# Kernel tuning notes

Hardware: AMD Instinct MI355X
Metric: run time of the kernel (lower is better)

The kernel has to match this reference:

```python
import jax, jax.numpy as jnp
import numpy as np

B, T, C = 4, 2048, 2048
H, HKV = 16, 4
D = C // H            # 128
G = H // HKV          # 4 query heads per kv head
ROPE_THETA = 10000.0


def _rope_tables(seq_len, head_dim, theta):
    inv = 1.0 / (theta ** (np.arange(0, head_dim, 2, dtype=np.float32) / head_dim))
    t = np.arange(seq_len, dtype=np.float32)
    f = np.outer(t, inv)  # (T, D/2)
    return jnp.asarray(np.cos(f)), jnp.asarray(np.sin(f))


def setup_inputs() -> dict:
    key = jax.random.key(0)
    ks = jax.random.split(key, 5)
    x = jax.random.normal(ks[0], (B, T, C), dtype=jnp.float32)
    W_q = jax.random.normal(ks[1], (H * D, C), dtype=jnp.float32) * 0.02
    W_k = jax.random.normal(ks[2], (HKV * D, C), dtype=jnp.float32) * 0.02
    W_v = jax.random.normal(ks[3], (HKV * D, C), dtype=jnp.float32) * 0.02
    W_o = jax.random.normal(ks[4], (C, C), dtype=jnp.float32) * 0.02
    cos, sin = _rope_tables(T, D, ROPE_THETA)
    return {"x": x, "W_q": W_q, "W_k": W_k, "W_v": W_v, "W_o": W_o,
            "cos": cos, "sin": sin}


def _apply_rope(xh, cos, sin):
    # xh: (B, h, T, D); cos/sin: (T, D/2)
    x0 = xh[..., 0::2]
    x1 = xh[..., 1::2]
    c = cos[None, None, :, :]
    s = sin[None, None, :, :]
    o0 = x0 * c - x1 * s
    o1 = x0 * s + x1 * c
    return jnp.stack([o0, o1], axis=-1).reshape(xh.shape)


def reference(x, W_q, W_k, W_v, W_o, cos, sin):
    b, t, c = x.shape
    q = (x @ W_q.T).reshape(b, t, H, D).transpose(0, 2, 1, 3)      # (B,H,T,D)
    k = (x @ W_k.T).reshape(b, t, HKV, D).transpose(0, 2, 1, 3)    # (B,HKV,T,D)
    v = (x @ W_v.T).reshape(b, t, HKV, D).transpose(0, 2, 1, 3)
    q = _apply_rope(q, cos[:t], sin[:t])
    k = _apply_rope(k, cos[:t], sin[:t])
    # GQA via reshape instead of repeat_interleave (same head ordering:
    # q head index h = kv*G + g).
    qg = q.reshape(b, HKV, G, t, D)
    scores = jnp.einsum('bkgtd,bksd->bkgts', qg, k) / jnp.sqrt(jnp.float32(D))
    causal = jnp.tril(jnp.ones((t, t), dtype=bool))
    scores = jnp.where(causal[None, None, None, :, :], scores, -jnp.inf)
    attn = jax.nn.softmax(scores, axis=-1)
    out = jnp.einsum('bkgts,bksd->bkgtd', attn, v)                 # (B,HKV,G,T,D)
    out = out.reshape(b, H, t, D).transpose(0, 2, 1, 3).reshape(b, t, c)
    return out @ W_o.T
```

## Files before the change

### kernel.cpp

```cpp
#include <hip/hip_runtime.h>
#include <cmath>

typedef __attribute__((ext_vector_type(8))) short bf16x8;
typedef __attribute__((ext_vector_type(4))) float f32x4;
typedef __attribute__((ext_vector_type(16))) float f32x16;
typedef unsigned short u16;

__device__ __forceinline__ u16 f2bf(float f) {
  union { float f; unsigned u; } x; x.f = f;
  return (u16)((x.u + 0x7FFFu + ((x.u >> 16) & 1u)) >> 16);
}

__device__ __forceinline__ unsigned cvtpk(float lo, float hi) {
  unsigned r;
  asm("v_cvt_pk_bf16_f32 %0, %1, %2" : "=v"(r) : "v"(lo), "v"(hi));
  return r;
}

__device__ __forceinline__ void gload_lds16(const void* g, void* l) {
  __builtin_amdgcn_global_load_lds((const __attribute__((address_space(1))) unsigned*)g,
                                   (__attribute__((address_space(3))) unsigned*)l,
                                   16, 0, 0);
}

__global__ __launch_bounds__(256) void cast_bf16_kernel(const float* __restrict__ in,
                                                        u16* __restrict__ out, long n) {
  long i = (long)blockIdx.x * blockDim.x + threadIdx.x;
  long stride = (long)gridDim.x * blockDim.x;
  for (long j = i * 4; j < n; j += stride * 4) {
    float4 v = *(const float4*)(in + j);
    ushort4 o;
    o.x = f2bf(v.x); o.y = f2bf(v.y); o.z = f2bf(v.z); o.w = f2bf(v.w);
    *(ushort4*)(out + j) = o;
  }
}

template <int EPI>
__global__ __launch_bounds__(512, 2) void gemm_bt256(const u16* __restrict__ A,
                                                     const u16* __restrict__ B,
                                                     void* __restrict__ outp,
                                                     int M, int N, int K,
                                                     const float* __restrict__ cosp,
                                                     const float* __restrict__ sinp,
                                                     float scale) {
  __shared__ u16 lds[65536];
  const int tid = threadIdx.x;
  const int lane = tid & 63;
  const int l16 = lane & 15, lhi = lane >> 4;
  const int w = tid >> 6;
  const int wr = w >> 2, wc = w & 3;
  const int m0 = blockIdx.y * 256;
  const int n0 = blockIdx.x * 256;

  f32x4 acc[8][4];
#pragma unroll
  for (int i = 0; i < 8; ++i)
#pragma unroll
    for (int j = 0; j < 4; ++j) acc[i][j] = (f32x4)0.0f;

  const int NT = K >> 6;

  auto stage = [&](int t, int buf) {
    const int k0 = t << 6;
    u16* Ad = lds + buf * 32768;
    u16* Bd = Ad + 16384;
#pragma unroll
    for (int j = 0; j < 4; ++j) {
      int c = tid + j * 512;
      int row = c >> 3;
      int sboff = ((c & 7) * 16) ^ ((row & 7) << 4);
      gload_lds16(A + (size_t)(m0 + row) * K + k0 + (sboff >> 1), Ad + (size_t)c * 8);
    }
#pragma unroll
    for (int j = 0; j < 4; ++j) {
      int c = tid + j * 512;
      int row = c >> 3;
      int sboff = ((c & 7) * 16) ^ ((row & 7) << 4);
      gload_lds16(B + (size_t)(n0 + row) * K + k0 + (sboff >> 1), Bd + (size_t)c * 8);
    }
  };

  stage(0, 0);
  stage(1, 1);

  for (int t = 0; t < NT; ++t) {
    const int cur = t & 1;
    if (t + 1 < NT) { asm volatile("s_waitcnt vmcnt(8)" ::: "memory"); }
    else            { asm volatile("s_waitcnt vmcnt(0)" ::: "memory"); }
    __builtin_amdgcn_s_barrier();
    const char* Ab = (const char*)(lds + cur * 32768);
    const char* Bb = (const char*)(lds + cur * 32768 + 16384);
#pragma unroll
    for (int qm = 0; qm < 2; ++qm)
#pragma unroll
      for (int qn = 0; qn < 2; ++qn) {
        bf16x8 af[4][2], bfr[2][2];
#pragma unroll
        for (int mi = 0; mi < 4; ++mi) {
          int ra = wr * 128 + qm * 64 + mi * 16 + l16;
#pragma unroll
          for (int kk = 0; kk < 2; ++kk)
            af[mi][kk] = *(const bf16x8*)(Ab + ra * 128 + ((kk * 64 + lhi * 16) ^ ((ra & 7) << 4)));
        }
#pragma unroll
        for (int ni = 0; ni < 2; ++ni) {
          int rb = wc * 64 + qn * 32 + ni * 16 + l16;
#pragma unroll
          for (int kk = 0; kk < 2; ++kk)
            bfr[ni][kk] = *(const bf16x8*)(Bb + rb * 128 + ((kk * 64 + lhi * 16) ^ ((rb & 7) << 4)));
        }
        __builtin_amdgcn_s_setprio(1);
#pragma unroll
        for (int kk = 0; kk < 2; ++kk)
#pragma unroll
          for (int mi = 0; mi < 4; ++mi)
#pragma unroll
            for (int ni = 0; ni < 2; ++ni)
              acc[qm * 4 + mi][qn * 2 + ni] = __builtin_amdgcn_mfma_f32_16x16x32_bf16(
                  af[mi][kk], bfr[ni][kk], acc[qm * 4 + mi][qn * 2 + ni], 0, 0, 0);
        __builtin_amdgcn_s_setprio(0);
      }
    asm volatile("s_waitcnt lgkmcnt(0)" ::: "memory");
    __builtin_amdgcn_s_barrier();
    if (t + 2 < NT) stage(t + 2, cur);
  }

  if (EPI == 2) {
    float* o = (float*)outp;
#pragma unroll
    for (int mi8 = 0; mi8 < 8; ++mi8)
#pragma unroll
      for (int r = 0; r < 4; ++r) {
        int row = m0 + wr * 128 + mi8 * 16 + lhi * 4 + r;
#pragma unroll
        for (int nj = 0; nj < 4; ++nj) {
          int col = n0 + wc * 64 + nj * 16 + l16;
          o[(size_t)row * N + col] = acc[mi8][nj][r];
        }
      }
  } else {
    u16* o = (u16*)outp;
    const int nheads = N >> 7;
#pragma unroll
    for (int mi8 = 0; mi8 < 8; ++mi8)
#pragma unroll
      for (int r = 0; r < 4; ++r) {
        int row = m0 + wr * 128 + mi8 * 16 + lhi * 4 + r;
        int b = row >> 11;
        int tt = row & 2047;
#pragma unroll
        for (int nj = 0; nj < 4; ++nj) {
          int col = n0 + wc * 64 + nj * 16 + l16;
          int hh = col >> 7, dd = col & 127;
          float v = acc[mi8][nj][r];
          float p = __shfl_xor(v, 1);
          float c = cosp[tt * 64 + (dd >> 1)];
          float s = sinp[tt * 64 + (dd >> 1)];
          v = (lane & 1) ? fmaf(p, s, v * c) : fmaf(v, c, -p * s);
          v *= scale;
          o[((size_t)(b * nheads + hh) * 2048 + tt) * 128 + dd] = f2bf(v);
        }
      }
  }
}

template <int EPI>
__global__ __launch_bounds__(256) void gemm_bt(const u16* __restrict__ A,
                                               const u16* __restrict__ B,
                                               void* __restrict__ outp,
                                               u16* __restrict__ vtp,
                                               int M, int N, int K,
                                               const float* __restrict__ cosp,
                                               const float* __restrict__ sinp,
                                               float scale) {
  __shared__ u16 As[128 * 64];
  __shared__ u16 Bs[128 * 64];
  const int tid = threadIdx.x;
  const int lane = tid & 63;
  const int l16 = lane & 15, lhi = lane >> 4;
  const int w = tid >> 6;
  const int wr = w >> 1, wc = w & 1;
  const int m0 = blockIdx.y * 128;
  const int n0 = blockIdx.x * 128;
  const int wbase = tid - lane;

  f32x4 acc[4][4];
#pragma unroll
  for (int i = 0; i < 4; ++i)
#pragma unroll
    for (int j = 0; j < 4; ++j) acc[i][j] = (f32x4)0.0f;

  for (int k0 = 0; k0 < K; k0 += 64) {
    __syncthreads();
#pragma unroll
    for (int j = 0; j < 4; ++j) {
      int c = tid + j * 256;
      gload_lds16(A + (size_t)(m0 + (c >> 3)) * K + k0 + (c & 7) * 8,
                  As + (size_t)(wbase + j * 256) * 8);
    }
#pragma unroll
    for (int j = 0; j < 4; ++j) {
      int c = tid + j * 256;
      gload_lds16(B + (size_t)(n0 + (c >> 3)) * K + k0 + (c & 7) * 8,
                  Bs + (size_t)(wbase + j * 256) * 8);
    }
    __syncthreads();
#pragma unroll
    for (int kk = 0; kk < 64; kk += 32) {
      bf16x8 af[4], bfr[4];
#pragma unroll
      for (int mi = 0; mi < 4; ++mi)
        af[mi] = *(const bf16x8*)&As[(wr * 64 + mi * 16 + l16) * 64 + kk + lhi * 8];
#pragma unroll
      for (int ni = 0; ni < 4; ++ni)
        bfr[ni] = *(const bf16x8*)&Bs[(wc * 64 + ni * 16 + l16) * 64 + kk + lhi * 8];
#pragma unroll
      for (int mi = 0; mi < 4; ++mi)
#pragma unroll
        for (int ni = 0; ni < 4; ++ni)
          acc[mi][ni] = __builtin_amdgcn_mfma_f32_16x16x32_bf16(af[mi], bfr[ni], acc[mi][ni], 0, 0, 0);
    }
  }

  {
    const int bx = blockIdx.x;
    if (bx < 4) {
      u16* o = (u16*)outp;
#pragma unroll
      for (int mi = 0; mi < 4; ++mi)
#pragma unroll
        for (int r = 0; r < 4; ++r) {
          int row = m0 + wr * 64 + mi * 16 + lhi * 4 + r;
          int b = row >> 11;
          int t = row & 2047;
          size_t base = ((size_t)(b * 4 + bx) * 2048 + t) * 128;
#pragma unroll
          for (int ni = 0; ni < 4; ++ni) {
            int d = wc * 64 + ni * 16 + l16;
            float v = acc[mi][ni][r];
            float p = __shfl_xor(v, 1);
            float c = cosp[t * 64 + (d >> 1)];
            float s = sinp[t * 64 + (d >> 1)];
            v = (lane & 1) ? fmaf(p, s, v * c) : fmaf(v, c, -p * s);
            o[base + d] = f2bf(v);
          }
        }
    } else {
      const int kvh = bx - 4;
#pragma unroll
      for (int mi = 0; mi < 4; ++mi)
#pragma unroll
        for (int r = 0; r < 4; ++r) {
          int row = m0 + wr * 64 + mi * 16 + lhi * 4 + r;
          int b = row >> 11;
          int t = row & 2047;
          size_t base = ((size_t)(b * 4 + kvh) * 128) * 2048 + t;
#pragma unroll
          for (int ni = 0; ni < 4; ++ni) {
            int d = wc * 64 + ni * 16 + l16;
            vtp[base + (size_t)d * 2048] = f2bf(acc[mi][ni][r]);
          }
        }
    }
  }
}

__global__ __launch_bounds__(256, 2) void attn_kernel(const u16* __restrict__ Q,
                                                      const u16* __restrict__ Kp,
                                                      const u16* __restrict__ Vtp,
                                                      u16* __restrict__ O) {
  __shared__ u16 lds[17408];
  u16* Ks  = lds;
  u16* VTs = lds + 8192;

  const int tid = threadIdx.x;
  const int lane = tid & 63;
  const int w = tid >> 6;
  const int l5 = lane & 31, hi = lane >> 5;
  const int bid = blockIdx.x;
  const int qt = 15 - (bid >> 6);
  const int hb = bid & 63;
  const int h = hb >> 2;
  const int b = hb & 3;
  const int kvh = h >> 2;
  const int q0 = qt * 128;
  const int wbase = tid - lane;
  const int wrow0 = q0 + w * 32;
  const int qg = wrow0 + l5;

  const u16* Qb = Q + ((size_t)((b * 16 + h) * 2048 + wrow0)) * 128;
  const u16* Kb = Kp + (size_t)(b * 4 + kvh) * 2048 * 128;
  const u16* Vtb = Vtp + (size_t)(b * 4 + kvh) * 128 * 2048;

  bf16x8 qf[8];
#pragma unroll
  for (int ks = 0; ks < 8; ++ks)
    qf[ks] = *(const bf16x8*)(Qb + (size_t)l5 * 128 + ks * 16 + hi * 8);

  f32x16 oacc[4];
#pragma unroll
  for (int i = 0; i < 4; ++i) oacc[i] = (f32x16)0.0f;
  float m = -3.0e38f, l = 0.0f;

  const int nkt = 2 * qt + 2;
  for (int kt = 0; kt < nkt; ++kt) {
    const int t0 = kt * 64;
    __syncthreads();
#pragma unroll
    for (int j = 0; j < 4; ++j) {
      int c = tid + j * 256;
      int row = c >> 4;
      int sboff = ((c & 15) * 16) ^ ((row & 15) << 4);
      gload_lds16(Kb + (size_t)(t0 + row) * 128 + (sboff >> 1),
                  Ks + (size_t)(wbase + j * 256) * 8);
    }
#pragma unroll
    for (int j = 0; j < 4; ++j) {
      int c = tid + j * 256;
      int d = c >> 3;
      int sboff = ((c & 7) * 16) ^ ((d & 7) << 4);
      gload_lds16(Vtb + (size_t)d * 2048 + t0 + (sboff >> 1),
                  VTs + (size_t)(wbase + j * 256) * 8);
    }
    __syncthreads();

    if (t0 <= wrow0 + 31) {
      float p[32];
      const char* ksb = (const char*)Ks;
#pragma unroll
      for (int kt2 = 0; kt2 < 2; ++kt2) {
        f32x16 sacc = (f32x16)0.0f;
        int row = kt2 * 32 + l5;
#pragma unroll
        for (int ks = 0; ks < 8; ++ks) {
          bf16x8 kf = *(const bf16x8*)(ksb + row * 256 + ((ks * 32 + hi * 16) ^ ((row & 15) << 4)));
          sacc = __builtin_amdgcn_mfma_f32_32x32x16_bf16(kf, qf[ks], sacc, 0, 0, 0);
        }
#pragma unroll
        for (int r = 0; r < 16; ++r) p[kt2 * 16 + r] = sacc[r];
      }

      if (t0 + 63 > wrow0) {
#pragma unroll
        for (int kt2 = 0; kt2 < 2; ++kt2)
#pragma unroll
          for (int r = 0; r < 16; ++r) {
            int kvg = t0 + kt2 * 32 + (r & 3) + 8 * (r >> 2) + 4 * hi;
            if (kvg > qg) p[kt2 * 16 + r] = -3.0e38f;
          }
      }

      float mx[16];
#pragma unroll
      for (int i = 0; i < 16; ++i) mx[i] = fmaxf(p[i], p[i + 16]);
#pragma unroll
      for (int i = 0; i < 8; ++i) mx[i] = fmaxf(mx[i], mx[i + 8]);
#pragma unroll
      for (int i = 0; i < 4; ++i) mx[i] = fmaxf(mx[i], mx[i + 4]);
      float rm = fmaxf(fmaxf(mx[0], mx[1]), fmaxf(mx[2], mx[3]));
      rm = fmaxf(rm, __shfl_xor(rm, 32));

      bool defer = __all(rm <= m + 8.0f);
      if (!defer) {
        float mnew = fmaxf(m, rm);
        float sc = exp2f(m - mnew);
        m = mnew;
        l *= sc;
#pragma unroll
        for (int i = 0; i < 4; ++i)
#pragma unroll
          for (int r = 0; r < 16; ++r) oacc[i][r] *= sc;
      }

#pragma unroll
      for (int i = 0; i < 32; ++i) p[i] = exp2f(p[i] - m);
      float sm[16];
#pragma unroll
      for (int i = 0; i < 16; ++i) sm[i] = p[i] + p[i + 16];
#pragma unroll
      for (int i = 0; i < 8; ++i) sm[i] += sm[i + 8];
#pragma unroll
      for (int i = 0; i < 4; ++i) sm[i] += sm[i + 4];
      float s2 = (sm[0] + sm[1]) + (sm[2] + sm[3]);
      s2 += __shfl_xor(s2, 32);
      l += s2;

      const char* vtb = (const char*)VTs;
#pragma unroll
      for (int kt2 = 0; kt2 < 2; ++kt2) {
#pragma unroll
        for (int sl = 0; sl < 2; ++sl) {
          int base = kt2 * 16 + sl * 8;
          unsigned A0 = cvtpk(p[base + 0], p[base + 1]);
          unsigned A1 = cvtpk(p[base + 2], p[base + 3]);
          unsigned A2 = cvtpk(p[base + 4], p[base + 5]);
          unsigned A3 = cvtpk(p[base + 6], p[base + 7]);
          unsigned XA0 = __shfl_xor(A0, 32);
          unsigned XA1 = __shfl_xor(A1, 32);
          unsigned XA2 = __shfl_xor(A2, 32);
          unsigned XA3 = __shfl_xor(A3, 32);
          union { unsigned u[4]; bf16x8 v; } pf;
          pf.u[0] = hi ? XA2 : A0;
          pf.u[1] = hi ? XA3 : A1;
          pf.u[2] = hi ? A2 : XA0;
          pf.u[3] = hi ? A3 : XA1;
          int s = kt2 * 2 + sl;
#pragma unroll
          for (int dt = 0; dt < 4; ++dt) {
            int row = dt * 32 + l5;
            bf16x8 vb = *(const bf16x8*)(vtb + row * 128 + ((s * 32 + hi * 16) ^ ((row & 7) << 4)));
            oacc[dt] = __builtin_amdgcn_mfma_f32_32x32x16_bf16(vb, pf.v, oacc[dt], 0, 0, 0);
          }
        }
      }
    }
  }

  float inv = 1.0f / l;
  __syncthreads();
  u16* OS = lds + w * 4352;
#pragma unroll
  for (int dt = 0; dt < 4; ++dt)
#pragma unroll
    for (int r = 0; r < 16; ++r) {
      int d = dt * 32 + (r & 3) + 8 * (r >> 2) + 4 * hi;
      OS[l5 * 136 + d] = f2bf(oacc[dt][r] * inv);
    }
  __syncthreads();
  u16* Ob = O + ((size_t)(b * 2048 + q0)) * 2048 + h * 128;
#pragma unroll
  for (int j = 0; j < 8; ++j) {
    int c = tid + j * 256;
    int row = c >> 4, col = c & 15;
    *(bf16x8*)(Ob + (size_t)row * 2048 + col * 8) =
        *(const bf16x8*)&lds[(row >> 5) * 4352 + (row & 31) * 136 + col * 8];
  }
}

extern "C" void kernel_launch(void* const* d_in, const int* in_sizes, int n_in,
                              void* d_out, int out_size, void* d_ws, size_t ws_size,
                              hipStream_t stream) {
  (void)in_sizes; (void)n_in; (void)out_size; (void)ws_size;
  const float* x    = (const float*)d_in[0];
  const float* Wq   = (const float*)d_in[1];
  const float* Wk   = (const float*)d_in[2];
  const float* Wv   = (const float*)d_in[3];
  const float* Wo   = (const float*)d_in[4];
  const float* cosp = (const float*)d_in[5];
  const float* sinp = (const float*)d_in[6];

  u16* ws  = (u16*)d_ws;
  u16* xbf = ws;
  u16* Wqb = xbf + 16777216;
  u16* Wkb = Wqb + 4194304;
  u16* Wvb = Wkb + 1048576;
  u16* Wob = Wvb + 1048576;
  u16* Qb  = Wob + 4194304;
  u16* Kb  = Qb + 16777216;
  u16* Vb  = Kb + 4194304;
  u16* AO  = xbf;

  cast_bf16_kernel<<<2048, 256, 0, stream>>>(x,  xbf, 16777216L);
  cast_bf16_kernel<<<512,  256, 0, stream>>>(Wq, Wqb, 4194304L);
  cast_bf16_kernel<<<256,  256, 0, stream>>>(Wk, Wkb, 1048576L);
  cast_bf16_kernel<<<256,  256, 0, stream>>>(Wv, Wvb, 1048576L);
  cast_bf16_kernel<<<512,  256, 0, stream>>>(Wo, Wob, 4194304L);

  const float qscale = (float)(1.4426950408889634 / sqrt(128.0));

  gemm_bt256<0><<<dim3(8, 32), 512, 0, stream>>>(xbf, Wqb, Qb, 8192, 2048, 2048, cosp, sinp, qscale);
  gemm_bt<3><<<dim3(8, 64), 256, 0, stream>>>(xbf, Wkb, Kb, Vb, 8192, 1024, 2048, cosp, sinp, 1.0f);

  attn_kernel<<<1024, 256, 0, stream>>>(Qb, Kb, Vb, AO);

  gemm_bt256<2><<<dim3(8, 32), 512, 0, stream>>>(AO, Wob, d_out, 8192, 2048, 2048, nullptr, nullptr, 1.0f);
}
```

Before: 338.7 us.

## Double-buffer K/V in attention, enlarge query tile, merge cast kernels

The attention kernel now uses 512 threads covering a 256-row query tile, so the block count is halved and each K/V tile loaded into LDS is shared by twice as many query rows. K/V tiles are double-buffered: the next tile is prefetched with global_load_lds while the current one is computed, using explicit vmcnt waits and barriers. The five fp32-to-bf16 cast launches are merged into one kernel that walks the contiguous workspace. The trade-offs are a larger LDS footprint, causal load imbalance over fewer and bigger blocks, and a branch per element in the cast loop.

```diff
diff --git a/kernel.cpp b/kernel.cpp
--- a/kernel.cpp
+++ b/kernel.cpp
@@ -23,12 +23,23 @@
                                    16, 0, 0);
 }
 
-__global__ __launch_bounds__(256) void cast_bf16_kernel(const float* __restrict__ in,
-                                                        u16* __restrict__ out, long n) {
+__global__ __launch_bounds__(256) void cast_all_kernel(const float* __restrict__ x,
+                                                       const float* __restrict__ wq,
+                                                       const float* __restrict__ wk,
+                                                       const float* __restrict__ wv,
+                                                       const float* __restrict__ wo,
+                                                       u16* __restrict__ out) {
+  const long b1 = 16777216, b2 = 20971520, b3 = 22020096, b4 = 23068672, b5 = 27262976;
   long i = (long)blockIdx.x * blockDim.x + threadIdx.x;
   long stride = (long)gridDim.x * blockDim.x;
-  for (long j = i * 4; j < n; j += stride * 4) {
-    float4 v = *(const float4*)(in + j);
+  for (long j = i * 4; j < b5; j += stride * 4) {
+    const float* src; long off;
+    if (j < b1)      { src = x;  off = j; }
+    else if (j < b2) { src = wq; off = j - b1; }
+    else if (j < b3) { src = wk; off = j - b2; }
+    else if (j < b4) { src = wv; off = j - b3; }
+    else             { src = wo; off = j - b4; }
+    float4 v = *(const float4*)(src + off);
     ushort4 o;
     o.x = f2bf(v.x); o.y = f2bf(v.y); o.z = f2bf(v.z); o.w = f2bf(v.w);
     *(ushort4*)(out + j) = o;
@@ -265,25 +276,23 @@
   }
 }
 
-__global__ __launch_bounds__(256, 2) void attn_kernel(const u16* __restrict__ Q,
+__global__ __launch_bounds__(512, 2) void attn_kernel(const u16* __restrict__ Q,
                                                       const u16* __restrict__ Kp,
                                                       const u16* __restrict__ Vtp,
                                                       u16* __restrict__ O) {
-  __shared__ u16 lds[17408];
-  u16* Ks  = lds;
-  u16* VTs = lds + 8192;
+  __shared__ u16 lds[32768];
 
   const int tid = threadIdx.x;
   const int lane = tid & 63;
   const int w = tid >> 6;
   const int l5 = lane & 31, hi = lane >> 5;
   const int bid = blockIdx.x;
-  const int qt = 15 - (bid >> 6);
+  const int qt = 7 - (bid >> 6);
   const int hb = bid & 63;
   const int h = hb >> 2;
   const int b = hb & 3;
   const int kvh = h >> 2;
-  const int q0 = qt * 128;
+  const int q0 = qt * 256;
   const int wbase = tid - lane;
   const int wrow0 = q0 + w * 32;
   const int qg = wrow0 + l5;
@@ -302,31 +311,48 @@
   for (int i = 0; i < 4; ++i) oacc[i] = (f32x16)0.0f;
   float m = -3.0e38f, l = 0.0f;
 
-  const int nkt = 2 * qt + 2;
+  const int nkt = 4 * qt + 4;
+
+  auto stageKV = [&](int kt, int buf) {
+    const int t0k = kt * 64;
+    u16* Kd = lds + buf * 8192;
+    u16* Vd = lds + 16384 + buf * 8192;
+#pragma unroll
+    for (int j = 0; j < 2; ++j) {
+      int c = tid + j * 512;
+      int row = c >> 4;
+      int sboff = ((c & 15) * 16) ^ ((row & 15) << 4);
+      gload_lds16(Kb + (size_t)(t0k + row) * 128 + (sboff >> 1),
+                  Kd + (size_t)(wbase + j * 512) * 8);
+    }
+#pragma unroll
+    for (int j = 0; j < 2; ++j) {
+      int c = tid + j * 512;
+      int d = c >> 3;
+      int sboff = ((c & 7) * 16) ^ ((d & 7) << 4);
+      gload_lds16(Vtb + (size_t)d * 2048 + t0k + (sboff >> 1),
+                  Vd + (size_t)(wbase + j * 512) * 8);
+    }
+  };
+
+  stageKV(0, 0);
+
   for (int kt = 0; kt < nkt; ++kt) {
     const int t0 = kt * 64;
-    __syncthreads();
-#pragma unroll
-    for (int j = 0; j < 4; ++j) {
-      int c = tid + j * 256;
-      int row = c >> 4;
-      int sboff = ((c & 15) * 16) ^ ((row & 15) << 4);
-      gload_lds16(Kb + (size_t)(t0 + row) * 128 + (sboff >> 1),
-                  Ks + (size_t)(wbase + j * 256) * 8);
-    }
-#pragma unroll
-    for (int j = 0; j < 4; ++j) {
-      int c = tid + j * 256;
-      int d = c >> 3;
-      int sboff = ((c & 7) * 16) ^ ((d & 7) << 4);
-      gload_lds16(Vtb + (size_t)d * 2048 + t0 + (sboff >> 1),
-                  VTs + (size_t)(wbase + j * 256) * 8);
-    }
-    __syncthreads();
+    const int cur = kt & 1;
+    if (kt + 1 < nkt) {
+      stageKV(kt + 1, cur ^ 1);
+      asm volatile("s_waitcnt vmcnt(4)" ::: "memory");
+    } else {
+      asm volatile("s_waitcnt vmcnt(0)" ::: "memory");
+    }
+    __builtin_amdgcn_s_barrier();
 
     if (t0 <= wrow0 + 31) {
+      const char* ksb = (const char*)(lds + cur * 8192);
+      const char* vtb = (const char*)(lds + 16384 + cur * 8192);
+
       float p[32];
-      const char* ksb = (const char*)Ks;
 #pragma unroll
       for (int kt2 = 0; kt2 < 2; ++kt2) {
         f32x16 sacc = (f32x16)0.0f;
@@ -385,7 +411,6 @@
       s2 += __shfl_xor(s2, 32);
       l += s2;
 
-      const char* vtb = (const char*)VTs;
 #pragma unroll
       for (int kt2 = 0; kt2 < 2; ++kt2) {
 #pragma unroll
@@ -414,26 +439,34 @@
         }
       }
     }
+
+    asm volatile("s_waitcnt lgkmcnt(0)" ::: "memory");
+    __builtin_amdgcn_s_barrier();
   }
 
   float inv = 1.0f / l;
   __syncthreads();
-  u16* OS = lds + w * 4352;
-#pragma unroll
-  for (int dt = 0; dt < 4; ++dt)
-#pragma unroll
-    for (int r = 0; r < 16; ++r) {
-      int d = dt * 32 + (r & 3) + 8 * (r >> 2) + 4 * hi;
-      OS[l5 * 136 + d] = f2bf(oacc[dt][r] * inv);
-    }
-  __syncthreads();
-  u16* Ob = O + ((size_t)(b * 2048 + q0)) * 2048 + h * 128;
-#pragma unroll
-  for (int j = 0; j < 8; ++j) {
-    int c = tid + j * 256;
-    int row = c >> 4, col = c & 15;
-    *(bf16x8*)(Ob + (size_t)row * 2048 + col * 8) =
-        *(const bf16x8*)&lds[(row >> 5) * 4352 + (row & 31) * 136 + col * 8];
+  for (int half = 0; half < 2; ++half) {
+    if ((w >> 2) == half) {
+      u16* OSw = lds + (w & 3) * 4352;
+#pragma unroll
+      for (int dt = 0; dt < 4; ++dt)
+#pragma unroll
+        for (int r = 0; r < 16; ++r) {
+          int d = dt * 32 + (r & 3) + 8 * (r >> 2) + 4 * hi;
+          OSw[l5 * 136 + d] = f2bf(oacc[dt][r] * inv);
+        }
+    }
+    __syncthreads();
+    u16* Ob = O + ((size_t)(b * 2048 + q0 + half * 128)) * 2048 + h * 128;
+#pragma unroll
+    for (int j = 0; j < 4; ++j) {
+      int c = tid + j * 512;
+      int row = c >> 4, col = c & 15;
+      *(bf16x8*)(Ob + (size_t)row * 2048 + col * 8) =
+          *(const bf16x8*)&lds[(row >> 5) * 4352 + (row & 31) * 136 + col * 8];
+    }
+    __syncthreads();
   }
 }
 
@@ -460,18 +493,14 @@
   u16* Vb  = Kb + 4194304;
   u16* AO  = xbf;
 
-  cast_bf16_kernel<<<2048, 256, 0, stream>>>(x,  xbf, 16777216L);
-  cast_bf16_kernel<<<512,  256, 0, stream>>>(Wq, Wqb, 4194304L);
-  cast_bf16_kernel<<<256,  256, 0, stream>>>(Wk, Wkb, 1048576L);
-  cast_bf16_kernel<<<256,  256, 0, stream>>>(Wv, Wvb, 1048576L);
-  cast_bf16_kernel<<<512,  256, 0, stream>>>(Wo, Wob, 4194304L);
+  cast_all_kernel<<<2048, 256, 0, stream>>>(x, Wq, Wk, Wv, Wo, ws);
 
   const float qscale = (float)(1.4426950408889634 / sqrt(128.0));
 
   gemm_bt256<0><<<dim3(8, 32), 512, 0, stream>>>(xbf, Wqb, Qb, 8192, 2048, 2048, cosp, sinp, qscale);
   gemm_bt<3><<<dim3(8, 64), 256, 0, stream>>>(xbf, Wkb, Kb, Vb, 8192, 1024, 2048, cosp, sinp, 1.0f);
 
-  attn_kernel<<<1024, 256, 0, stream>>>(Qb, Kb, Vb, AO);
+  attn_kernel<<<512, 512, 0, stream>>>(Qb, Kb, Vb, AO);
 
   gemm_bt256<2><<<dim3(8, 32), 512, 0, stream>>>(AO, Wob, d_out, 8192, 2048, 2048, nullptr, nullptr, 1.0f);
 }
```

Result: faster. 324.5 us (-4.2%).
